# Kernel tuning notes

Measured on AMD Instinct MI355X. Metric: run time of the kernel, lower is better.

The kernel has to match this reference:

```python
import jax, jax.numpy as jnp
import numpy as np

N = 100000
E = 1600000
IN_C = 128
OUT_C = 32
BN_EPS = 1e-5


def setup_inputs() -> dict:
    key = jax.random.key(0)
    k1, k2, k3, k4, k5, k6 = jax.random.split(key, 6)
    x = jax.random.normal(k1, (N, IN_C), dtype=jnp.float32)
    edge_index = jax.random.randint(k2, (2, E), 0, N, dtype=jnp.int64)
    # GCNConv linear weight (glorot-ish) and bias
    W = jax.random.normal(k3, (IN_C, OUT_C), dtype=jnp.float32) / np.sqrt(IN_C)
    b = jax.random.normal(k4, (OUT_C,), dtype=jnp.float32) * 0.01
    # BatchNorm1d affine params
    gamma = jnp.ones((OUT_C,), dtype=jnp.float32) + 0.1 * jax.random.normal(k5, (OUT_C,), dtype=jnp.float32)
    beta = 0.1 * jax.random.normal(k6, (OUT_C,), dtype=jnp.float32)
    return {"x": x, "edge_index": edge_index, "W": W, "b": b, "gamma": gamma, "beta": beta}


def reference(x, edge_index, W, b, gamma, beta):
    # --- GCNConv (PyG semantics): add self-loops, sym degree norm, linear ---
    self_loops = jnp.arange(N, dtype=edge_index.dtype)
    row = jnp.concatenate([edge_index[0], self_loops])  # source nodes [E+N]
    col = jnp.concatenate([edge_index[1], self_loops])  # target nodes [E+N]

    deg = jax.ops.segment_sum(jnp.ones_like(col, dtype=x.dtype), col, num_segments=N)
    deg_inv_sqrt = jnp.where(deg > 0, jax.lax.rsqrt(deg), 0.0)
    norm = deg_inv_sqrt[row] * deg_inv_sqrt[col]  # [E+N]

    h = x @ W  # project first (PyG order): [N, OUT_C]
    msgs = norm[:, None] * h[row]  # gather + scale: [E+N, OUT_C]
    out = jax.ops.segment_sum(msgs, col, num_segments=N) + b  # scatter-add

    # --- BatchNorm1d (training mode: batch statistics, biased variance) ---
    mean = jnp.mean(out, axis=0)
    var = jnp.mean((out - mean) ** 2, axis=0)
    y = (out - mean) * jax.lax.rsqrt(var + BN_EPS) * gamma + beta
    return y
```

## Files before the change

kernel.cpp:

```cpp
#include <hip/hip_runtime.h>
#include <hip/hip_fp16.h>

#define IN_C  128
#define OUT_C 32
#define BN_EPS 1e-5f
#define BKT_BITS 7
#define BKT 128
#define C_CAP 2816
#define CH  6144

typedef float floatx4 __attribute__((ext_vector_type(4)));

__global__ void zero_kernel(int* __restrict__ bcnt, float* __restrict__ sums) {
    int i = threadIdx.x;
    if (i < 1024) bcnt[i] = 0;
    if (i < 512) sums[i] = 0.0f;
}

__global__ __launch_bounds__(512) void binfill_kernel(
    const int* __restrict__ row, const int* __restrict__ col,
    int* __restrict__ bcnt, int* __restrict__ adjp, int E)
{
    __shared__ int pk[CH];
    __shared__ unsigned short bk[CH];
    __shared__ int h[1024];
    __shared__ int excl[1024];
    __shared__ int lcur[1024];
    __shared__ int basg[1024];
    __shared__ int wsum[8];
    const int t  = threadIdx.x;
    const int e0 = blockIdx.x * CH;
    const int n  = min(CH, E - e0);

    for (int i = t; i < 1024; i += 512) h[i] = 0;
    __syncthreads();

    int myb[12], myp[12];
    #pragma unroll
    for (int k = 0; k < 12; ++k) {
        int i = t + 512 * k;
        myb[k] = -1;
        if (i < n) {
            int c = col[e0 + i];
            int r = row[e0 + i];
            myb[k] = c >> BKT_BITS;
            myp[k] = (r << BKT_BITS) | (c & (BKT - 1));
            atomicAdd(&h[myb[k]], 1);
        }
    }
    __syncthreads();

    {
        const int lane = t & 63;
        int a  = h[2 * t];
        int b2 = h[2 * t + 1];
        int s = a + b2;
        int incl = s;
        #pragma unroll
        for (int d = 1; d < 64; d <<= 1) {
            int u = __shfl_up(incl, d);
            if (lane >= d) incl += u;
        }
        if (lane == 63) wsum[t >> 6] = incl;
        __syncthreads();
        int wpre = 0;
        #pragma unroll
        for (int w = 0; w < 7; ++w) wpre += (w < (t >> 6)) ? wsum[w] : 0;
        int pre = wpre + incl - s;

        excl[2 * t] = pre;          lcur[2 * t] = pre;
        excl[2 * t + 1] = pre + a;  lcur[2 * t + 1] = pre + a;
        int g0 = 0, g1 = 0;
        if (a)  { g0 = atomicAdd(&bcnt[2 * t], a);      if (g0 > C_CAP - a)  g0 = max(0, C_CAP - a); }
        if (b2) { g1 = atomicAdd(&bcnt[2 * t + 1], b2); if (g1 > C_CAP - b2) g1 = max(0, C_CAP - b2); }
        basg[2 * t]     = (2 * t) * C_CAP + g0;
        basg[2 * t + 1] = (2 * t + 1) * C_CAP + g1;
    }
    __syncthreads();

    #pragma unroll
    for (int k = 0; k < 12; ++k) {
        if (myb[k] >= 0) {
            int b = myb[k];
            int l = atomicAdd(&lcur[b], 1);
            pk[l] = myp[k];
            bk[l] = (unsigned short)b;
        }
    }
    __syncthreads();

    for (int i = t; i < n; i += 512) {
        int b = bk[i];
        adjp[basg[b] + (i - excl[b])] = pk[i];
    }
}

__global__ __launch_bounds__(256) void sort_kernel(
    const int* __restrict__ bcnt, int* __restrict__ adjp,
    int* __restrict__ counts, int2* __restrict__ ord2, int N)
{
    __shared__ int eL[C_CAP];
    __shared__ int h[BKT];
    __shared__ int cur[BKT];
    __shared__ int wdeg[BKT];
    __shared__ int eoff[BKT];
    __shared__ int wv[2];
    const int t = threadIdx.x;
    const int b = blockIdx.x;
    const int s0  = b * C_CAP;
    const int cnt = min(bcnt[b], C_CAP);
    const int base = b << BKT_BITS;

    if (t < BKT) h[t] = 0;
    __syncthreads();
    for (int i = t; i < cnt; i += 256) {
        int p = adjp[s0 + i];
        eL[i] = p;
        atomicAdd(&h[p & (BKT - 1)], 1);
    }
    __syncthreads();

    if (t < BKT) {
        const int lane = t & 63;
        int v = h[t];
        int incl = v;
        #pragma unroll
        for (int d = 1; d < 64; d <<= 1) {
            int u = __shfl_up(incl, d);
            if (lane >= d) incl += u;
        }
        if (lane == 63) wv[t >> 6] = incl;
        int e = incl - v;
        eoff[t] = e;
    }
    __syncthreads();
    if (t < BKT) {
        int e = eoff[t] + ((t >= 64) ? wv[0] : 0);
        eoff[t] = e;
        cur[t] = e;
        int nd = base + t;
        if (nd < N) counts[nd] = h[t];
        wdeg[t] = (nd < N) ? h[t] : -1;
    }
    __syncthreads();

    if (t < BKT) {
        int w0 = t & ~31;
        int my = wdeg[t];
        int rank = 0;
        #pragma unroll
        for (int j = 0; j < 32; ++j) {
            int dj = wdeg[w0 + j];
            rank += (dj < my) || (dj == my && (w0 + j) < t);
        }
        int slot = base + w0 + rank;
        if (my >= 0) {
            unsigned pack = ((unsigned)(s0 + eoff[t]) << 8) | (unsigned)min(h[t], 255);
            ord2[slot] = make_int2((int)pack, base + t);
        } else {
            ord2[slot] = make_int2(0, -1);
        }
    }
    __syncthreads();

    for (int i = t; i < cnt; i += 256) {
        int p = eL[i];
        int pos = atomicAdd(&cur[p & (BKT - 1)], 1);
        adjp[s0 + pos] = p >> BKT_BITS;
    }
}

__global__ __launch_bounds__(256) void gemm_kernel(
    const float* __restrict__ x, const float* __restrict__ W,
    const int* __restrict__ counts, __half* __restrict__ gh0,
    __half* __restrict__ gh1, int N)
{
    __shared__ float xs[32 * 132];
    __shared__ float wl[128 * 32];
    const int tid = threadIdx.x;
    const int r0  = blockIdx.x * 32;

    #pragma unroll
    for (int k = 0; k < 4; ++k) {
        int idx = tid + 256 * k;
        int row = idx >> 5;
        int c4  = idx & 31;
        int rr  = r0 + row;
        float4 v = make_float4(0.f, 0.f, 0.f, 0.f);
        if (rr < N) v = reinterpret_cast<const float4*>(x)[(size_t)rr * 32 + c4];
        *reinterpret_cast<float4*>(&xs[row * 132 + c4 * 4]) = v;
    }
    #pragma unroll
    for (int k = 0; k < 4; ++k) {
        int idx = tid + 256 * k;
        reinterpret_cast<float4*>(wl)[idx] = reinterpret_cast<const float4*>(W)[idx];
    }
    __syncthreads();

    const int r_local = tid >> 3;
    const int c4 = (tid & 7) * 4;
    float4 sum = make_float4(0.f, 0.f, 0.f, 0.f);
    #pragma unroll 8
    for (int k = 0; k < 128; ++k) {
        float  xv = xs[r_local * 132 + k];
        float4 w4 = *reinterpret_cast<const float4*>(&wl[k * 32 + c4]);
        sum.x = fmaf(xv, w4.x, sum.x);
        sum.y = fmaf(xv, w4.y, sum.y);
        sum.z = fmaf(xv, w4.z, sum.z);
        sum.w = fmaf(xv, w4.w, sum.w);
    }
    const int r = r0 + r_local;
    if (r < N) {
        float dis = rsqrtf((float)counts[r] + 1.0f);
        union { __half2 h[2]; float2 f; } u;
        u.h[0] = __floats2half2_rn(sum.x * dis, sum.y * dis);
        u.h[1] = __floats2half2_rn(sum.z * dis, sum.w * dis);
        __half* tb = (c4 < 16) ? gh0 : gh1;
        reinterpret_cast<float2*>(tb)[(size_t)r * 4 + ((c4 & 15) >> 2)] = u.f;
    }
}

__global__ __launch_bounds__(256, 8) void pull_kernel(
    const int2* __restrict__ ord2, const int* __restrict__ adjp,
    const __half* __restrict__ gh0, const __half* __restrict__ gh1,
    float* __restrict__ out, int NW)
{
    const int xcd  = blockIdx.x & 7;
    const int half = xcd >> 2;
    const int stride = (gridDim.x >> 3) * 4;

    const int t   = threadIdx.x;
    const int grp = t >> 3;
    const int way = (t >> 1) & 3;
    const int cl  = t & 1;
    const float4* g4 = reinterpret_cast<const float4*>(half ? gh1 : gh0);

    const int NWP = (NW + 1) >> 1;
    for (int idx = (blockIdx.x >> 3) * 4 + (xcd & 3); idx < NWP; idx += stride) {
        const int win = idx * 2 + (grp >> 4);
        if (win >= NW) continue;
        const int q = grp & 15;
        const int2 o0 = ord2[win * 32 + q];
        const int2 o1 = ord2[win * 32 + 31 - q];
        const int n0 = o0.y, n1 = o1.y;
        const unsigned p0 = (unsigned)o0.x, p1 = (unsigned)o1.x;
        const int len0 = (int)(p0 & 255u), s0 = (int)(p0 >> 8);
        const int len1 = (int)(p1 & 255u), s1 = (int)(p1 >> 8);
        const int total = len0 + len1;
        const int s1m = s1 - len0;

        float a00=0.f,a01=0.f,a02=0.f,a03=0.f,a04=0.f,a05=0.f,a06=0.f,a07=0.f;
        float a10=0.f,a11=0.f,a12=0.f,a13=0.f,a14=0.f,a15=0.f,a16=0.f,a17=0.f;

        #define UNPK(Vv) \
            __half2 h0 = *reinterpret_cast<const __half2*>(&(Vv).x); \
            __half2 h1 = *reinterpret_cast<const __half2*>(&(Vv).y); \
            __half2 h2 = *reinterpret_cast<const __half2*>(&(Vv).z); \
            __half2 h3 = *reinterpret_cast<const __half2*>(&(Vv).w); \
            float2 u0 = __half22float2(h0), u1 = __half22float2(h1); \
            float2 u2 = __half22float2(h2), u3 = __half22float2(h3); \
            float f0 = u0.x, f1 = u0.y, f2 = u1.x, f3 = u1.y; \
            float f4 = u2.x, f5 = u2.y, f6 = u3.x, f7 = u3.y;

        if (way == 0 && n0 >= 0) {
            float4 sv = g4[(size_t)n0 * 2 + cl];
            UNPK(sv)
            a00=f0; a01=f1; a02=f2; a03=f3; a04=f4; a05=f5; a06=f6; a07=f7;
        } else if (way == 1 && n1 >= 0) {
            float4 sv = g4[(size_t)n1 * 2 + cl];
            UNPK(sv)
            a10=f0; a11=f1; a12=f2; a13=f3; a14=f4; a15=f5; a16=f6; a17=f7;
        }

        #define LDI(kk) __builtin_nontemporal_load(&adjp[(((kk) < len0) ? s0 : s1m) + (kk)])
        #define ACC2(Vv, s) { \
            UNPK(Vv) \
            a00 += (s) ? f0 : 0.f;  a10 += (s) ? 0.f : f0; \
            a01 += (s) ? f1 : 0.f;  a11 += (s) ? 0.f : f1; \
            a02 += (s) ? f2 : 0.f;  a12 += (s) ? 0.f : f2; \
            a03 += (s) ? f3 : 0.f;  a13 += (s) ? 0.f : f3; \
            a04 += (s) ? f4 : 0.f;  a14 += (s) ? 0.f : f4; \
            a05 += (s) ? f5 : 0.f;  a15 += (s) ? 0.f : f5; \
            a06 += (s) ? f6 : 0.f;  a16 += (s) ? 0.f : f6; \
            a07 += (s) ? f7 : 0.f;  a17 += (s) ? 0.f : f7; }

        int k = way;
        for (; k + 12 < total; k += 16) {
            int e0 = LDI(k);
            int e1 = LDI(k + 4);
            int e2 = LDI(k + 8);
            int e3 = LDI(k + 12);
            float4 w0 = g4[(size_t)e0 * 2 + cl];
            float4 w1 = g4[(size_t)e1 * 2 + cl];
            float4 w2 = g4[(size_t)e2 * 2 + cl];
            float4 w3 = g4[(size_t)e3 * 2 + cl];
            { ACC2(w0, k      < len0) }
            { ACC2(w1, k + 4  < len0) }
            { ACC2(w2, k + 8  < len0) }
            { ACC2(w3, k + 12 < len0) }
        }
        for (; k < total; k += 4) {
            int e0 = LDI(k);
            float4 w0 = g4[(size_t)e0 * 2 + cl];
            { ACC2(w0, k < len0) }
        }
        #undef ACC2
        #undef LDI
        #undef UNPK

        #define RED(a) a += __shfl_xor(a, 2); a += __shfl_xor(a, 4);
        RED(a00) RED(a01) RED(a02) RED(a03) RED(a04) RED(a05) RED(a06) RED(a07)
        RED(a10) RED(a11) RED(a12) RED(a13) RED(a14) RED(a15) RED(a16) RED(a17)
        #undef RED

        if (way == 0 && n0 >= 0) {
            float dis = rsqrtf((float)len0 + 1.0f);
            floatx4 v0, v1;
            v0.x = a00 * dis; v0.y = a01 * dis; v0.z = a02 * dis; v0.w = a03 * dis;
            v1.x = a04 * dis; v1.y = a05 * dis; v1.z = a06 * dis; v1.w = a07 * dis;
            size_t ob = (size_t)n0 * 8 + half * 4 + cl * 2;
            __builtin_nontemporal_store(v0, &reinterpret_cast<floatx4*>(out)[ob]);
            __builtin_nontemporal_store(v1, &reinterpret_cast<floatx4*>(out)[ob + 1]);
        } else if (way == 1 && n1 >= 0) {
            float dis = rsqrtf((float)len1 + 1.0f);
            floatx4 v0, v1;
            v0.x = a10 * dis; v0.y = a11 * dis; v0.z = a12 * dis; v0.w = a13 * dis;
            v1.x = a14 * dis; v1.y = a15 * dis; v1.z = a16 * dis; v1.w = a17 * dis;
            size_t ob = (size_t)n1 * 8 + half * 4 + cl * 2;
            __builtin_nontemporal_store(v0, &reinterpret_cast<floatx4*>(out)[ob]);
            __builtin_nontemporal_store(v1, &reinterpret_cast<floatx4*>(out)[ob + 1]);
        }
    }
}

__global__ __launch_bounds__(256) void stats_kernel(
    const float* __restrict__ out, float* __restrict__ sums, long long n4)
{
    __shared__ float4 r1[256];
    __shared__ float4 r2[256];
    const int t = threadIdx.x;
    float4 ls = make_float4(0.f, 0.f, 0.f, 0.f);
    float4 lq = make_float4(0.f, 0.f, 0.f, 0.f);
    for (long long i = (long long)blockIdx.x * 256 + t; i < n4; i += (long long)gridDim.x * 256) {
        float4 v = reinterpret_cast<const float4*>(out)[i];
        ls.x += v.x; ls.y += v.y; ls.z += v.z; ls.w += v.w;
        lq.x = fmaf(v.x, v.x, lq.x); lq.y = fmaf(v.y, v.y, lq.y);
        lq.z = fmaf(v.z, v.z, lq.z); lq.w = fmaf(v.w, v.w, lq.w);
    }
    r1[t] = ls; r2[t] = lq;
    __syncthreads();
    #pragma unroll
    for (int off = 128; off >= 8; off >>= 1) {
        if (t < off) {
            float4 u1 = r1[t + off], u2 = r2[t + off];
            float4 v1 = r1[t],       v2 = r2[t];
            v1.x += u1.x; v1.y += u1.y; v1.z += u1.z; v1.w += u1.w;
            v2.x += u2.x; v2.y += u2.y; v2.z += u2.z; v2.w += u2.w;
            r1[t] = v1; r2[t] = v2;
        }
        __syncthreads();
    }
    if (t < 8) {
        float4 v1 = r1[t], v2 = r2[t];
        float* sb = sums + (blockIdx.x & 7) * 64;
        int cb = t * 4;
        atomicAdd(&sb[cb + 0], v1.x); atomicAdd(&sb[cb + 1], v1.y);
        atomicAdd(&sb[cb + 2], v1.z); atomicAdd(&sb[cb + 3], v1.w);
        atomicAdd(&sb[32 + cb + 0], v2.x); atomicAdd(&sb[32 + cb + 1], v2.y);
        atomicAdd(&sb[32 + cb + 2], v2.z); atomicAdd(&sb[32 + cb + 3], v2.w);
    }
}

__global__ __launch_bounds__(256) void bn_apply_kernel(
    float* __restrict__ out, const float* __restrict__ sums,
    const float* __restrict__ gamma, const float* __restrict__ beta,
    int N, long long n4)
{
    __shared__ float ssl[64];
    const int t = threadIdx.x;
    if (t < 32) {
        float s = 0.f, q = 0.f;
        #pragma unroll
        for (int r = 0; r < 8; ++r) { s += sums[r * 64 + t]; q += sums[r * 64 + 32 + t]; }
        float invN  = 1.0f / (float)N;
        float mean  = s * invN;
        float var   = q * invN - mean * mean;
        float scale = gamma[t] * rsqrtf(var + BN_EPS);
        ssl[t]      = scale;
        ssl[32 + t] = fmaf(-mean, scale, beta[t]);
    }
    __syncthreads();

    long long i = (long long)blockIdx.x * blockDim.x + t;
    if (i < n4) {
        int c4 = (int)(i & 7) * 4;
        float4 v = reinterpret_cast<float4*>(out)[i];
        v.x = fmaf(v.x, ssl[c4 + 0], ssl[32 + c4 + 0]);
        v.y = fmaf(v.y, ssl[c4 + 1], ssl[32 + c4 + 1]);
        v.z = fmaf(v.z, ssl[c4 + 2], ssl[32 + c4 + 2]);
        v.w = fmaf(v.w, ssl[c4 + 3], ssl[32 + c4 + 3]);
        reinterpret_cast<float4*>(out)[i] = v;
    }
}

extern "C" void kernel_launch(void* const* d_in, const int* in_sizes, int n_in,
                              void* d_out, int out_size, void* d_ws, size_t ws_size,
                              hipStream_t stream)
{
    const float* x     = (const float*)d_in[0];
    const int*   ei    = (const int*)d_in[1];
    const float* W     = (const float*)d_in[2];
    const float* gamma = (const float*)d_in[4];
    const float* beta  = (const float*)d_in[5];
    float* out = (float*)d_out;

    const int N = in_sizes[0] / IN_C;
    const int E = in_sizes[1] / 2;
    const int* row = ei;
    const int* col = ei + E;
    const int NB = (N + BKT - 1) >> BKT_BITS;

    __half* gh0   = (__half*)d_ws;
    __half* gh1   = gh0 + (size_t)N * 16;
    float* sums   = (float*)(gh1 + (size_t)N * 16);
    int*   counts = (int*)(sums + 576);
    int*   bcnt   = counts + N;
    int2*  ord2   = (int2*)(bcnt + 1024);
    int*   adjp   = (int*)(ord2 + (size_t)NB * BKT);

    zero_kernel   <<<1, 1024, 0, stream>>>(bcnt, sums);
    binfill_kernel<<<(E + CH - 1) / CH, 512, 0, stream>>>(row, col, bcnt, adjp, E);
    sort_kernel   <<<NB, 256, 0, stream>>>(bcnt, adjp, counts, ord2, N);

    gemm_kernel   <<<(N + 31) / 32, 256, 0, stream>>>(x, W, counts, gh0, gh1, N);

    const int NW = NB * 4;
    pull_kernel   <<<2048, 256, 0, stream>>>(ord2, adjp, gh0, gh1, out, NW);

    long long n4 = (long long)N * OUT_C / 4;
    stats_kernel  <<<1024, 256, 0, stream>>>(out, sums, n4);
    bn_apply_kernel<<<(int)((n4 + 255) / 256), 256, 0, stream>>>(out, sums, gamma, beta, N, n4);
}
```

Before: 125.6 us.

## Use 2 lanes per node pair with deeper gather unroll in pull kernel

Each node pair in the pull aggregation is now handled by 4 threads (2 ways × 2 column lanes) instead of 8, so each block covers four windows per iteration instead of two. The main loop issues 8 independent neighbor gathers per iteration instead of 4, and the shuffle reduction drops one step. This aims to cut reduction and lane-idle overhead on short adjacency lists and raise memory-level parallelism per thread. In exchange, registers per thread rise, so launch bounds drop to 4 blocks per CU, which may lower occupancy, and per-thread serial work on long lists increases.

```diff
diff --git a/kernel.cpp b/kernel.cpp
--- a/kernel.cpp
+++ b/kernel.cpp
@@ -220,7 +220,7 @@
     }
 }
 
-__global__ __launch_bounds__(256, 8) void pull_kernel(
+__global__ __launch_bounds__(256, 4) void pull_kernel(
     const int2* __restrict__ ord2, const int* __restrict__ adjp,
     const __half* __restrict__ gh0, const __half* __restrict__ gh1,
     float* __restrict__ out, int NW)
@@ -230,14 +230,14 @@
     const int stride = (gridDim.x >> 3) * 4;
 
     const int t   = threadIdx.x;
-    const int grp = t >> 3;
-    const int way = (t >> 1) & 3;
+    const int grp = t >> 2;
+    const int way = (t >> 1) & 1;
     const int cl  = t & 1;
     const float4* g4 = reinterpret_cast<const float4*>(half ? gh1 : gh0);
 
-    const int NWP = (NW + 1) >> 1;
-    for (int idx = (blockIdx.x >> 3) * 4 + (xcd & 3); idx < NWP; idx += stride) {
-        const int win = idx * 2 + (grp >> 4);
+    const int NWQ = (NW + 3) >> 2;
+    for (int idx = (blockIdx.x >> 3) * 4 + (xcd & 3); idx < NWQ; idx += stride) {
+        const int win = idx * 4 + (grp >> 4);
         if (win >= NW) continue;
         const int q = grp & 15;
         const int2 o0 = ord2[win * 32 + q];
@@ -285,21 +285,47 @@
             a07 += (s) ? f7 : 0.f;  a17 += (s) ? 0.f : f7; }
 
         int k = way;
-        for (; k + 12 < total; k += 16) {
+        for (; k + 14 < total; k += 16) {
             int e0 = LDI(k);
-            int e1 = LDI(k + 4);
-            int e2 = LDI(k + 8);
-            int e3 = LDI(k + 12);
+            int e1 = LDI(k + 2);
+            int e2 = LDI(k + 4);
+            int e3 = LDI(k + 6);
+            int e4 = LDI(k + 8);
+            int e5 = LDI(k + 10);
+            int e6 = LDI(k + 12);
+            int e7 = LDI(k + 14);
+            float4 w0 = g4[(size_t)e0 * 2 + cl];
+            float4 w1 = g4[(size_t)e1 * 2 + cl];
+            float4 w2 = g4[(size_t)e2 * 2 + cl];
+            float4 w3 = g4[(size_t)e3 * 2 + cl];
+            float4 w4 = g4[(size_t)e4 * 2 + cl];
+            float4 w5 = g4[(size_t)e5 * 2 + cl];
+            float4 w6 = g4[(size_t)e6 * 2 + cl];
+            float4 w7 = g4[(size_t)e7 * 2 + cl];
+            { ACC2(w0, k      < len0) }
+            { ACC2(w1, k + 2  < len0) }
+            { ACC2(w2, k + 4  < len0) }
+            { ACC2(w3, k + 6  < len0) }
+            { ACC2(w4, k + 8  < len0) }
+            { ACC2(w5, k + 10 < len0) }
+            { ACC2(w6, k + 12 < len0) }
+            { ACC2(w7, k + 14 < len0) }
+        }
+        for (; k + 6 < total; k += 8) {
+            int e0 = LDI(k);
+            int e1 = LDI(k + 2);
+            int e2 = LDI(k + 4);
+            int e3 = LDI(k + 6);
             float4 w0 = g4[(size_t)e0 * 2 + cl];
             float4 w1 = g4[(size_t)e1 * 2 + cl];
             float4 w2 = g4[(size_t)e2 * 2 + cl];
             float4 w3 = g4[(size_t)e3 * 2 + cl];
             { ACC2(w0, k      < len0) }
-            { ACC2(w1, k + 4  < len0) }
-            { ACC2(w2, k + 8  < len0) }
-            { ACC2(w3, k + 12 < len0) }
-        }
-        for (; k < total; k += 4) {
+            { ACC2(w1, k + 2  < len0) }
+            { ACC2(w2, k + 4  < len0) }
+            { ACC2(w3, k + 6  < len0) }
+        }
+        for (; k < total; k += 2) {
             int e0 = LDI(k);
             float4 w0 = g4[(size_t)e0 * 2 + cl];
             { ACC2(w0, k < len0) }
@@ -308,7 +334,7 @@
         #undef LDI
         #undef UNPK
 
-        #define RED(a) a += __shfl_xor(a, 2); a += __shfl_xor(a, 4);
+        #define RED(a) a += __shfl_xor(a, 2);
         RED(a00) RED(a01) RED(a02) RED(a03) RED(a04) RED(a05) RED(a06) RED(a07)
         RED(a10) RED(a11) RED(a12) RED(a13) RED(a14) RED(a15) RED(a16) RED(a17)
         #undef RED
```

Result: no change. 127.2 us (+1.2%).

## Fuse BatchNorm statistics accumulation into pull kernel, drop stats kernel

Applied to the files above, without the earlier changes.

Per-channel sum and sum-of-squares are now accumulated in registers inside the aggregation kernel, reduced across the wavefront and block, and atomically added into the sums buffer. The separate stats pass, which reread the whole output array, is removed. The pull kernel's occupancy hint drops from 8 to 6 to make room for the 16 extra accumulator registers. This saves a full read of the output and one launch, at the cost of possible register pressure and reduced occupancy in the gather-heavy kernel.

```diff
diff --git a/kernel.cpp b/kernel.cpp
--- a/kernel.cpp
+++ b/kernel.cpp
@@ -220,20 +220,24 @@
     }
 }
 
-__global__ __launch_bounds__(256, 8) void pull_kernel(
+__global__ __launch_bounds__(256, 6) void pull_kernel(
     const int2* __restrict__ ord2, const int* __restrict__ adjp,
     const __half* __restrict__ gh0, const __half* __restrict__ gh1,
-    float* __restrict__ out, int NW)
+    float* __restrict__ out, float* __restrict__ sums, int NW)
 {
     const int xcd  = blockIdx.x & 7;
     const int half = xcd >> 2;
     const int stride = (gridDim.x >> 3) * 4;
 
+    __shared__ float lds[4][2][16];
     const int t   = threadIdx.x;
     const int grp = t >> 3;
     const int way = (t >> 1) & 3;
     const int cl  = t & 1;
     const float4* g4 = reinterpret_cast<const float4*>(half ? gh1 : gh0);
+
+    float bn0=0.f,bn1=0.f,bn2=0.f,bn3=0.f,bn4=0.f,bn5=0.f,bn6=0.f,bn7=0.f;
+    float bq0=0.f,bq1=0.f,bq2=0.f,bq3=0.f,bq4=0.f,bq5=0.f,bq6=0.f,bq7=0.f;
 
     const int NWP = (NW + 1) >> 1;
     for (int idx = (blockIdx.x >> 3) * 4 + (xcd & 3); idx < NWP; idx += stride) {
@@ -321,6 +325,12 @@
             size_t ob = (size_t)n0 * 8 + half * 4 + cl * 2;
             __builtin_nontemporal_store(v0, &reinterpret_cast<floatx4*>(out)[ob]);
             __builtin_nontemporal_store(v1, &reinterpret_cast<floatx4*>(out)[ob + 1]);
+            bn0 += v0.x; bn1 += v0.y; bn2 += v0.z; bn3 += v0.w;
+            bn4 += v1.x; bn5 += v1.y; bn6 += v1.z; bn7 += v1.w;
+            bq0 = fmaf(v0.x, v0.x, bq0); bq1 = fmaf(v0.y, v0.y, bq1);
+            bq2 = fmaf(v0.z, v0.z, bq2); bq3 = fmaf(v0.w, v0.w, bq3);
+            bq4 = fmaf(v1.x, v1.x, bq4); bq5 = fmaf(v1.y, v1.y, bq5);
+            bq6 = fmaf(v1.z, v1.z, bq6); bq7 = fmaf(v1.w, v1.w, bq7);
         } else if (way == 1 && n1 >= 0) {
             float dis = rsqrtf((float)len1 + 1.0f);
             floatx4 v0, v1;
@@ -329,45 +339,35 @@
             size_t ob = (size_t)n1 * 8 + half * 4 + cl * 2;
             __builtin_nontemporal_store(v0, &reinterpret_cast<floatx4*>(out)[ob]);
             __builtin_nontemporal_store(v1, &reinterpret_cast<floatx4*>(out)[ob + 1]);
-        }
-    }
-}
-
-__global__ __launch_bounds__(256) void stats_kernel(
-    const float* __restrict__ out, float* __restrict__ sums, long long n4)
-{
-    __shared__ float4 r1[256];
-    __shared__ float4 r2[256];
-    const int t = threadIdx.x;
-    float4 ls = make_float4(0.f, 0.f, 0.f, 0.f);
-    float4 lq = make_float4(0.f, 0.f, 0.f, 0.f);
-    for (long long i = (long long)blockIdx.x * 256 + t; i < n4; i += (long long)gridDim.x * 256) {
-        float4 v = reinterpret_cast<const float4*>(out)[i];
-        ls.x += v.x; ls.y += v.y; ls.z += v.z; ls.w += v.w;
-        lq.x = fmaf(v.x, v.x, lq.x); lq.y = fmaf(v.y, v.y, lq.y);
-        lq.z = fmaf(v.z, v.z, lq.z); lq.w = fmaf(v.w, v.w, lq.w);
-    }
-    r1[t] = ls; r2[t] = lq;
-    __syncthreads();
-    #pragma unroll
-    for (int off = 128; off >= 8; off >>= 1) {
-        if (t < off) {
-            float4 u1 = r1[t + off], u2 = r2[t + off];
-            float4 v1 = r1[t],       v2 = r2[t];
-            v1.x += u1.x; v1.y += u1.y; v1.z += u1.z; v1.w += u1.w;
-            v2.x += u2.x; v2.y += u2.y; v2.z += u2.z; v2.w += u2.w;
-            r1[t] = v1; r2[t] = v2;
-        }
-        __syncthreads();
-    }
-    if (t < 8) {
-        float4 v1 = r1[t], v2 = r2[t];
-        float* sb = sums + (blockIdx.x & 7) * 64;
-        int cb = t * 4;
-        atomicAdd(&sb[cb + 0], v1.x); atomicAdd(&sb[cb + 1], v1.y);
-        atomicAdd(&sb[cb + 2], v1.z); atomicAdd(&sb[cb + 3], v1.w);
-        atomicAdd(&sb[32 + cb + 0], v2.x); atomicAdd(&sb[32 + cb + 1], v2.y);
-        atomicAdd(&sb[32 + cb + 2], v2.z); atomicAdd(&sb[32 + cb + 3], v2.w);
+            bn0 += v0.x; bn1 += v0.y; bn2 += v0.z; bn3 += v0.w;
+            bn4 += v1.x; bn5 += v1.y; bn6 += v1.z; bn7 += v1.w;
+            bq0 = fmaf(v0.x, v0.x, bq0); bq1 = fmaf(v0.y, v0.y, bq1);
+            bq2 = fmaf(v0.z, v0.z, bq2); bq3 = fmaf(v0.w, v0.w, bq3);
+            bq4 = fmaf(v1.x, v1.x, bq4); bq5 = fmaf(v1.y, v1.y, bq5);
+            bq6 = fmaf(v1.z, v1.z, bq6); bq7 = fmaf(v1.w, v1.w, bq7);
+        }
+    }
+
+    #define RED(a) a += __shfl_xor(a, 2); a += __shfl_xor(a, 4); \
+                   a += __shfl_xor(a, 8); a += __shfl_xor(a, 16); a += __shfl_xor(a, 32);
+    RED(bn0) RED(bn1) RED(bn2) RED(bn3) RED(bn4) RED(bn5) RED(bn6) RED(bn7)
+    RED(bq0) RED(bq1) RED(bq2) RED(bq3) RED(bq4) RED(bq5) RED(bq6) RED(bq7)
+    #undef RED
+    const int lane = t & 63, wv = t >> 6;
+    if (lane < 2) {
+        float* d = lds[wv][lane];
+        d[0]=bn0; d[1]=bn1; d[2]=bn2; d[3]=bn3; d[4]=bn4; d[5]=bn5; d[6]=bn6; d[7]=bn7;
+        d[8]=bq0; d[9]=bq1; d[10]=bq2; d[11]=bq3; d[12]=bq4; d[13]=bq5; d[14]=bq6; d[15]=bq7;
+    }
+    __syncthreads();
+    if (t < 32) {
+        int stat = t >> 4;
+        int ch   = t & 15;
+        int c2   = ch >> 3;
+        int j    = ch & 7;
+        float v = lds[0][c2][stat * 8 + j] + lds[1][c2][stat * 8 + j]
+                + lds[2][c2][stat * 8 + j] + lds[3][c2][stat * 8 + j];
+        atomicAdd(&sums[(blockIdx.x & 7) * 64 + stat * 32 + half * 16 + ch], v);
     }
 }
 
@@ -435,9 +435,8 @@
     gemm_kernel   <<<(N + 31) / 32, 256, 0, stream>>>(x, W, counts, gh0, gh1, N);
 
     const int NW = NB * 4;
-    pull_kernel   <<<2048, 256, 0, stream>>>(ord2, adjp, gh0, gh1, out, NW);
+    pull_kernel   <<<2048, 256, 0, stream>>>(ord2, adjp, gh0, gh1, out, sums, NW);
 
     long long n4 = (long long)N * OUT_C / 4;
-    stats_kernel  <<<1024, 256, 0, stream>>>(out, sums, n4);
     bn_apply_kernel<<<(int)((n4 + 255) / 256), 256, 0, stream>>>(out, sums, gamma, beta, N, n4);
 }
```

New measurement: 113.7 us, median of 2. 9.5% less time.
